# Performance work log

Hardware: AMD Instinct MI355X
Metric: run time of the kernel (lower is better)

## Reference

```python
import jax, jax.numpy as jnp
import numpy as np

H = 16
D_MODEL = 1024
D_K = D_MODEL // H  # 64
TEMP = float(np.sqrt(D_K))


def setup_inputs() -> dict:
    key = jax.random.key(0)
    ks = jax.random.split(key, 12)
    N = 2048
    s_in = 1.0 / np.sqrt(D_MODEL)
    inp = {
        "query": jax.random.normal(ks[0], (N, D_MODEL), jnp.float32),
        "key": jax.random.normal(ks[1], (N, D_MODEL), jnp.float32),
        "value": jax.random.normal(ks[2], (N, D_MODEL), jnp.float32),
        "Wq": jax.random.normal(ks[3], (D_MODEL, D_MODEL), jnp.float32) * s_in,
        "bq": jnp.zeros((D_MODEL,), jnp.float32),
        "Wk": jax.random.normal(ks[4], (D_MODEL, D_MODEL), jnp.float32) * s_in,
        "bk": jnp.zeros((D_MODEL,), jnp.float32),
        "Wv": jax.random.normal(ks[5], (D_MODEL, D_MODEL), jnp.float32) * s_in,
        "bv": jnp.zeros((D_MODEL,), jnp.float32),
        "Wo": jax.random.normal(ks[6], (D_MODEL, D_MODEL), jnp.float32) * s_in,
        "bo": jnp.zeros((D_MODEL,), jnp.float32),
    }
    return inp


def reference(query, key, value, Wq, bq, Wk, bk, Wv, bv, Wo, bo):
    # Project then split heads exactly like view(-1, h, d_k).transpose(0, 1):
    # (N, d_model) -> (N, h, d_k) -> (h, N, d_k)
    q = (query @ Wq + bq).reshape(-1, H, D_K).transpose(1, 0, 2)
    k = (key @ Wk + bk).reshape(-1, H, D_K).transpose(1, 0, 2)
    v = (value @ Wv + bv).reshape(-1, H, D_K).transpose(1, 0, 2)
    # Scaled dot-product attention (dropout is inference-mode identity)
    scores = jnp.einsum("hnd,hmd->hnm", q / TEMP, k)  # (h, N, N)
    attn = jax.nn.softmax(scores, axis=-1)
    x = jnp.einsum("hnm,hmd->hnd", attn, v)  # (h, N, d_k)
    x = x.transpose(1, 0, 2).reshape(-1, H * D_K)  # (N, d_model)
    out = x @ Wo + bo
    return (out, attn)
```

## Files before the change

### kernel.cpp

```cpp
#include <hip/hip_runtime.h>
#include <math.h>

#define NTOK 2048
#define DMODEL 1024
#define NHEAD 16
#define DHEAD 64
#define NTIL (NTOK / 64)

typedef _Float16 f16x8 __attribute__((ext_vector_type(8)));
typedef _Float16 f16x4 __attribute__((ext_vector_type(4)));
typedef _Float16 f16x2 __attribute__((ext_vector_type(2)));
typedef float f32x4 __attribute__((ext_vector_type(4)));
typedef float f32x16 __attribute__((ext_vector_type(16)));

union U32H2 { f16x2 h; unsigned u; };
union U8 { f16x8 v; unsigned u[4]; };

__device__ __forceinline__ void split16(float x, _Float16& hi, _Float16& lo) {
    hi = (_Float16)x;
    lo = (_Float16)(x - (float)hi);
}
__device__ __forceinline__ unsigned packh(_Float16 a, _Float16 b) {
    U32H2 c; c.h = f16x2{a, b}; return c.u;
}

__global__ void __launch_bounds__(256) prep_w_kernel(
        const float* __restrict__ Wq, const float* __restrict__ Wk,
        const float* __restrict__ Wv, const float* __restrict__ Wo,
        _Float16* __restrict__ Wt) {
    __shared__ float T[32][33];
    const int z = blockIdx.z;
    const float* W = (z == 0) ? Wq : (z == 1) ? Wk : (z == 2) ? Wv : Wo;
    _Float16* Whi = Wt + (size_t)z * 2 * 1024 * 1024;
    _Float16* Wlo = Whi + (size_t)1024 * 1024;
    const int t = threadIdx.x;
    const int k0 = blockIdx.y * 32, n0 = blockIdx.x * 32;
    const int r = t >> 3, c4 = (t & 7) * 4;
    const float4 v = *(const float4*)(W + (size_t)(k0 + r) * DMODEL + n0 + c4);
    T[r][c4 + 0] = v.x; T[r][c4 + 1] = v.y; T[r][c4 + 2] = v.z; T[r][c4 + 3] = v.w;
    __syncthreads();
    f16x4 hv, lv;
#pragma unroll
    for (int j = 0; j < 4; ++j) {
        _Float16 h, l;
        split16(T[c4 + j][r], h, l);
        hv[j] = h; lv[j] = l;
    }
    *(f16x4*)(Whi + (size_t)(n0 + r) * DMODEL + k0 + c4) = hv;
    *(f16x4*)(Wlo + (size_t)(n0 + r) * DMODEL + k0 + c4) = lv;
}

__global__ void __launch_bounds__(256) prep_a_kernel(
        const float* __restrict__ q, const float* __restrict__ k, const float* __restrict__ v,
        _Float16* __restrict__ As) {
    const int z = blockIdx.y;
    const float* A = (z == 0) ? q : (z == 1) ? k : v;
    const size_t PL = (size_t)NTOK * DMODEL;
    _Float16* H = As + (size_t)z * 2 * PL;
    _Float16* L = H + PL;
    const size_t off = ((size_t)blockIdx.x * 256 + threadIdx.x) * 8;
    const float4 a = *(const float4*)(A + off);
    const float4 b = *(const float4*)(A + off + 4);
    f16x8 hv, lv; _Float16 h, lo;
    split16(a.x, h, lo); hv[0] = h; lv[0] = lo;
    split16(a.y, h, lo); hv[1] = h; lv[1] = lo;
    split16(a.z, h, lo); hv[2] = h; lv[2] = lo;
    split16(a.w, h, lo); hv[3] = h; lv[3] = lo;
    split16(b.x, h, lo); hv[4] = h; lv[4] = lo;
    split16(b.y, h, lo); hv[5] = h; lv[5] = lo;
    split16(b.z, h, lo); hv[6] = h; lv[6] = lo;
    split16(b.w, h, lo); hv[7] = h; lv[7] = lo;
    *(f16x8*)(H + off) = hv;
    *(f16x8*)(L + off) = lv;
}

__global__ void __launch_bounds__(256) qkv_mfma_kernel(
        const _Float16* __restrict__ As,
        const _Float16* __restrict__ Wt,
        const float* __restrict__ bq, const float* __restrict__ bk, const float* __restrict__ bv,
        _Float16* __restrict__ Qh, _Float16* __restrict__ Ql,
        _Float16* __restrict__ Kh, _Float16* __restrict__ Vth) {
    __shared__ _Float16 Ah[64][40], Al[64][40], Bh[128][40], Bl[128][40];
    const int z = blockIdx.z;
    const size_t PL = (size_t)NTOK * DMODEL;
    const _Float16* AH = As + (size_t)z * 2 * PL;
    const _Float16* AL = AH + PL;
    const _Float16* WH = Wt + (size_t)z * 2 * 1024 * 1024;
    const _Float16* WL = WH + (size_t)1024 * 1024;
    const float* bias = (z == 0) ? bq : (z == 1) ? bk : bv;

    const int t = threadIdx.x;
    const int l = t & 63, wid = t >> 6;
    const int lr = l & 15, lk = l >> 4;
    const int m0 = blockIdx.y * 64, n0 = blockIdx.x * 128;
    const int wm = (wid >> 1) * 32, wn = (wid & 1) * 64;

    f32x4 acc[2][4];
#pragma unroll
    for (int mi = 0; mi < 2; ++mi)
#pragma unroll
        for (int ni = 0; ni < 4; ++ni)
#pragma unroll
            for (int e = 0; e < 4; ++e) acc[mi][ni][e] = 0.f;

    for (int k0 = 0; k0 < DMODEL; k0 += 32) {
        __syncthreads();
        {
            const int r = t >> 2, c8 = (t & 3) * 8;
            *(f16x8*)&Ah[r][c8] = *(const f16x8*)(AH + (size_t)(m0 + r) * DMODEL + k0 + c8);
            *(f16x8*)&Al[r][c8] = *(const f16x8*)(AL + (size_t)(m0 + r) * DMODEL + k0 + c8);
        }
#pragma unroll
        for (int p = 0; p < 2; ++p) {
            const int idx = t + p * 256;
            const int r = idx >> 2, c8 = (idx & 3) * 8;
            *(f16x8*)&Bh[r][c8] = *(const f16x8*)(WH + (size_t)(n0 + r) * DMODEL + k0 + c8);
            *(f16x8*)&Bl[r][c8] = *(const f16x8*)(WL + (size_t)(n0 + r) * DMODEL + k0 + c8);
        }
        __syncthreads();

        f16x8 ah[2], al[2], bh[4], bl[4];
#pragma unroll
        for (int i = 0; i < 2; ++i) {
            ah[i] = *(f16x8*)&Ah[wm + i * 16 + lr][lk * 8];
            al[i] = *(f16x8*)&Al[wm + i * 16 + lr][lk * 8];
        }
#pragma unroll
        for (int i = 0; i < 4; ++i) {
            bh[i] = *(f16x8*)&Bh[wn + i * 16 + lr][lk * 8];
            bl[i] = *(f16x8*)&Bl[wn + i * 16 + lr][lk * 8];
        }
        __builtin_amdgcn_s_setprio(1);
#pragma unroll
        for (int mi = 0; mi < 2; ++mi)
#pragma unroll
            for (int ni = 0; ni < 4; ++ni) {
                acc[mi][ni] = __builtin_amdgcn_mfma_f32_16x16x32_f16(ah[mi], bh[ni], acc[mi][ni], 0, 0, 0);
                acc[mi][ni] = __builtin_amdgcn_mfma_f32_16x16x32_f16(ah[mi], bl[ni], acc[mi][ni], 0, 0, 0);
                acc[mi][ni] = __builtin_amdgcn_mfma_f32_16x16x32_f16(al[mi], bh[ni], acc[mi][ni], 0, 0, 0);
            }
        __builtin_amdgcn_s_setprio(0);
    }

#pragma unroll
    for (int ni = 0; ni < 4; ++ni) {
        const int col = n0 + wn + ni * 16 + lr;
        const float bv_ = bias[col];
#pragma unroll
        for (int mi = 0; mi < 2; ++mi) {
            if (z == 2) {
                f16x4 hv;
#pragma unroll
                for (int i = 0; i < 4; ++i) hv[i] = (_Float16)(acc[mi][ni][i] + bv_);
                const int row = m0 + wm + mi * 16 + lk * 4;
                *(f16x4*)(Vth + (size_t)col * NTOK + row) = hv;
            } else {
#pragma unroll
                for (int i = 0; i < 4; ++i) {
                    const int row = m0 + wm + mi * 16 + lk * 4 + i;
                    float v = acc[mi][ni][i] + bv_;
                    if (z == 0) {
                        v *= 0.125f;
                        _Float16 h, lo;
                        split16(v, h, lo);
                        Qh[(size_t)row * DMODEL + col] = h;
                        Ql[(size_t)row * DMODEL + col] = lo;
                    } else {
                        Kh[(size_t)row * DMODEL + col] = (_Float16)v;
                    }
                }
            }
        }
    }
}

__global__ void __launch_bounds__(256, 2) fused_attn_kernel(
        const _Float16* __restrict__ Qh, const _Float16* __restrict__ Ql,
        const _Float16* __restrict__ Kh, const _Float16* __restrict__ Vth,
        float* __restrict__ attn, float* __restrict__ Xp) {
    __shared__ _Float16 KB[4][64][64];
    __shared__ _Float16 VB[4][64][64];
    const int t = threadIdx.x, l = t & 63, w = t >> 6, q = l & 31, h = l >> 5;
    const int hh = blockIdx.y;
    const int rw = blockIdx.x * 128 + w * 32;
    const int sr = t >> 3, sc = t & 7;
    const int qrow = rw + q;

    f16x8 qbh[4], qbl[4];
#pragma unroll
    for (int s = 0; s < 4; ++s) {
        const size_t off = (size_t)qrow * DMODEL + hh * DHEAD + s * 16 + h * 8;
        qbh[s] = *(const f16x8*)(Qh + off);
        qbl[s] = *(const f16x8*)(Ql + off);
    }

    auto stageK = [&](int buf, int j0) {
#pragma unroll
        for (int p = 0; p < 2; ++p) {
            const int r = sr + p * 32; const int cs = (sc ^ (r & 7)) * 8;
            *(f16x8*)&KB[buf][r][cs] = *(const f16x8*)(Kh + (size_t)(j0 + r) * DMODEL + hh * DHEAD + sc * 8);
        }
    };
    auto stageV = [&](int buf, int j0) {
#pragma unroll
        for (int p = 0; p < 2; ++p) {
            const int r = sr + p * 32; const int cs = (sc ^ (r & 7)) * 8;
            *(f16x8*)&VB[buf][r][cs] = *(const f16x8*)(Vth + (size_t)(hh * DHEAD + r) * NTOK + j0 + sc * 8);
        }
    };

    auto qkt = [&](int buf, f32x16 (&c)[2]) {
#pragma unroll
        for (int kb = 0; kb < 2; ++kb) {
#pragma unroll
            for (int r = 0; r < 16; ++r) c[kb][r] = 0.f;
            __builtin_amdgcn_s_setprio(1);
#pragma unroll
            for (int s = 0; s < 4; ++s) {
                const int rk = kb * 32 + q; const int cc = ((2 * s + h) ^ (rk & 7)) * 8;
                const f16x8 ah = *(f16x8*)&KB[buf][rk][cc];
                c[kb] = __builtin_amdgcn_mfma_f32_32x32x16_f16(ah, qbh[s], c[kb], 0, 0, 0);
                c[kb] = __builtin_amdgcn_mfma_f32_32x32x16_f16(ah, qbl[s], c[kb], 0, 0, 0);
            }
            __builtin_amdgcn_s_setprio(0);
        }
    };

    float lsum = 0.f;
    stageK(0, 0);
    stageK(1, 64);
    for (int it = 0; it < NTIL; it += 2) {
        __syncthreads();
        if (it + 2 < NTIL) stageK((it + 2) & 3, (it + 2) * 64);
        if (it + 3 < NTIL) stageK((it + 3) & 3, (it + 3) * 64);
#pragma unroll
        for (int u = 0; u < 2; ++u) {
            f32x16 c[2];
            qkt((it + u) & 3, c);
#pragma unroll
            for (int kb = 0; kb < 2; ++kb)
#pragma unroll
                for (int r = 0; r < 16; ++r) lsum += __expf(c[kb][r]);
        }
    }
    lsum += __shfl_xor(lsum, 32);
    const float linv = 1.f / lsum;

    f32x16 x0, x1;
#pragma unroll
    for (int r = 0; r < 16; ++r) { x0[r] = 0.f; x1[r] = 0.f; }

    __syncthreads();
    stageK(0, 0);  stageV(0, 0);
    stageK(1, 64); stageV(1, 64);
    for (int it = 0; it < NTIL; it += 2) {
        __syncthreads();
        if (it + 2 < NTIL) { stageK((it + 2) & 3, (it + 2) * 64); stageV((it + 2) & 3, (it + 2) * 64); }
        if (it + 3 < NTIL) { stageK((it + 3) & 3, (it + 3) * 64); stageV((it + 3) & 3, (it + 3) * 64); }
#pragma unroll
        for (int u = 0; u < 2; ++u) {
            const int cur = (it + u) & 3;
            const int j0 = (it + u) * 64;
            f32x16 c[2];
            qkt(cur, c);

#pragma unroll
            for (int kb = 0; kb < 2; ++kb) {
                float p[16];
#pragma unroll
                for (int r = 0; r < 16; ++r) p[r] = __expf(c[kb][r]) * linv;

                const int kbase = j0 + kb * 32;
#pragma unroll
                for (int i = 0; i < 4; ++i) {
                    f32x4 st;
                    st[0] = p[4 * i]; st[1] = p[4 * i + 1]; st[2] = p[4 * i + 2]; st[3] = p[4 * i + 3];
                    *(f32x4*)(attn + ((size_t)hh * NTOK + qrow) * NTOK + kbase + 8 * i + 4 * h) = st;
                }

                _Float16 hf[16];
#pragma unroll
                for (int r = 0; r < 16; ++r) hf[r] = (_Float16)p[r];
                unsigned ph[8];
#pragma unroll
                for (int i = 0; i < 8; ++i) ph[i] = packh(hf[2 * i], hf[2 * i + 1]);

#pragma unroll
                for (int ss = 0; ss < 2; ++ss) {
                    const int b = 4 * ss;
                    const unsigned eh0 = __shfl_xor(h ? ph[b + 0] : ph[b + 2], 32);
                    const unsigned eh1 = __shfl_xor(h ? ph[b + 1] : ph[b + 3], 32);
                    U8 pah;
                    pah.u[0] = h ? eh0 : ph[b + 0]; pah.u[1] = h ? eh1 : ph[b + 1];
                    pah.u[2] = h ? ph[b + 2] : eh0; pah.u[3] = h ? ph[b + 3] : eh1;
                    const int ks = kb * 2 + ss;
                    __builtin_amdgcn_s_setprio(1);
                    {
                        const int rd0 = q; const int cv0 = ((2 * ks + h) ^ (rd0 & 7)) * 8;
                        const f16x8 vh = *(f16x8*)&VB[cur][rd0][cv0];
                        x0 = __builtin_amdgcn_mfma_f32_32x32x16_f16(pah.v, vh, x0, 0, 0, 0);
                    }
                    {
                        const int rd1 = 32 + q; const int cv1 = ((2 * ks + h) ^ (rd1 & 7)) * 8;
                        const f16x8 vh = *(f16x8*)&VB[cur][rd1][cv1];
                        x1 = __builtin_amdgcn_mfma_f32_32x32x16_f16(pah.v, vh, x1, 0, 0, 0);
                    }
                    __builtin_amdgcn_s_setprio(0);
                }
            }
        }
    }

#pragma unroll
    for (int r = 0; r < 16; ++r) {
        const int qloc = (r & 3) + 8 * (r >> 2) + 4 * h;
        Xp[(size_t)(rw + qloc) * DMODEL + hh * DHEAD + q]      = x0[r];
        Xp[(size_t)(rw + qloc) * DMODEL + hh * DHEAD + 32 + q] = x1[r];
    }
}

__global__ void __launch_bounds__(256) out_mfma_kernel(
        const float* __restrict__ Xp,
        const _Float16* __restrict__ WH, const _Float16* __restrict__ WL,
        const float* __restrict__ bo, float* __restrict__ out) {
    __shared__ _Float16 Ah[64][40], Al[64][40], Bh[128][40], Bl[128][40];
    const int t = threadIdx.x;
    const int l = t & 63, wid = t >> 6;
    const int lr = l & 15, lk = l >> 4;
    const int m0 = blockIdx.y * 64, n0 = blockIdx.x * 128;
    const int wm = (wid >> 1) * 32, wn = (wid & 1) * 64;

    f32x4 acc[2][4];
#pragma unroll
    for (int mi = 0; mi < 2; ++mi)
#pragma unroll
        for (int ni = 0; ni < 4; ++ni)
#pragma unroll
            for (int e = 0; e < 4; ++e) acc[mi][ni][e] = 0.f;

    for (int k0 = 0; k0 < DMODEL; k0 += 32) {
        __syncthreads();
#pragma unroll
        for (int p = 0; p < 2; ++p) {
            const int idx = t + p * 256;
            const int r = idx >> 3, c4 = (idx & 7) * 4;
            const size_t off = (size_t)(m0 + r) * DMODEL + k0 + c4;
            const float4 v0 = *(const float4*)(Xp + off);
            f16x4 hv, lv; _Float16 h, lo;
            split16(v0.x, h, lo); hv[0] = h; lv[0] = lo;
            split16(v0.y, h, lo); hv[1] = h; lv[1] = lo;
            split16(v0.z, h, lo); hv[2] = h; lv[2] = lo;
            split16(v0.w, h, lo); hv[3] = h; lv[3] = lo;
            *(f16x4*)&Ah[r][c4] = hv;
            *(f16x4*)&Al[r][c4] = lv;
        }
#pragma unroll
        for (int p = 0; p < 2; ++p) {
            const int idx = t + p * 256;
            const int r = idx >> 2, c8 = (idx & 3) * 8;
            *(f16x8*)&Bh[r][c8] = *(const f16x8*)(WH + (size_t)(n0 + r) * DMODEL + k0 + c8);
            *(f16x8*)&Bl[r][c8] = *(const f16x8*)(WL + (size_t)(n0 + r) * DMODEL + k0 + c8);
        }
        __syncthreads();

        f16x8 ah[2], al[2], bh[4], bl[4];
#pragma unroll
        for (int i = 0; i < 2; ++i) {
            ah[i] = *(f16x8*)&Ah[wm + i * 16 + lr][lk * 8];
            al[i] = *(f16x8*)&Al[wm + i * 16 + lr][lk * 8];
        }
#pragma unroll
        for (int i = 0; i < 4; ++i) {
            bh[i] = *(f16x8*)&Bh[wn + i * 16 + lr][lk * 8];
            bl[i] = *(f16x8*)&Bl[wn + i * 16 + lr][lk * 8];
        }
        __builtin_amdgcn_s_setprio(1);
#pragma unroll
        for (int mi = 0; mi < 2; ++mi)
#pragma unroll
            for (int ni = 0; ni < 4; ++ni) {
                acc[mi][ni] = __builtin_amdgcn_mfma_f32_16x16x32_f16(ah[mi], bh[ni], acc[mi][ni], 0, 0, 0);
                acc[mi][ni] = __builtin_amdgcn_mfma_f32_16x16x32_f16(ah[mi], bl[ni], acc[mi][ni], 0, 0, 0);
                acc[mi][ni] = __builtin_amdgcn_mfma_f32_16x16x32_f16(al[mi], bh[ni], acc[mi][ni], 0, 0, 0);
            }
        __builtin_amdgcn_s_setprio(0);
    }

#pragma unroll
    for (int ni = 0; ni < 4; ++ni) {
        const int col = n0 + wn + ni * 16 + lr;
        const float bv_ = bo[col];
#pragma unroll
        for (int mi = 0; mi < 2; ++mi)
#pragma unroll
            for (int i = 0; i < 4; ++i) {
                const int row = m0 + wm + mi * 16 + lk * 4 + i;
                out[(size_t)row * DMODEL + col] = acc[mi][ni][i] + bv_;
            }
    }
}

extern "C" void kernel_launch(void* const* d_in, const int* in_sizes, int n_in,
                              void* d_out, int out_size, void* d_ws, size_t ws_size,
                              hipStream_t stream) {
    (void)in_sizes; (void)n_in; (void)out_size; (void)ws_size;
    const float* query = (const float*)d_in[0];
    const float* key_  = (const float*)d_in[1];
    const float* value = (const float*)d_in[2];
    const float* Wq = (const float*)d_in[3];
    const float* bq = (const float*)d_in[4];
    const float* Wk = (const float*)d_in[5];
    const float* bk = (const float*)d_in[6];
    const float* Wv = (const float*)d_in[7];
    const float* bv = (const float*)d_in[8];
    const float* Wo = (const float*)d_in[9];
    const float* bo = (const float*)d_in[10];

    float* out  = (float*)d_out;
    float* attn = out + (size_t)NTOK * DMODEL;

    const size_t MM = (size_t)1024 * 1024;
    _Float16* ws16 = (_Float16*)d_ws;
    _Float16* Wt  = ws16;
    _Float16* Qh  = ws16 + 8 * MM;
    _Float16* Ql  = Qh  + 2 * MM;
    _Float16* Kh_ = Ql  + 2 * MM;
    _Float16* Vth = Kh_ + 2 * MM;

    float* Xp = (float*)ws16;

    _Float16* As = (_Float16*)attn;

    dim3 blk(256);
    prep_w_kernel<<<dim3(32, 32, 4), blk, 0, stream>>>(Wq, Wk, Wv, Wo, Wt);
    prep_a_kernel<<<dim3(1024, 3), blk, 0, stream>>>(query, key_, value, As);
    qkv_mfma_kernel<<<dim3(8, 32, 3), blk, 0, stream>>>(As, Wt, bq, bk, bv,
                                                        Qh, Ql, Kh_, Vth);
    fused_attn_kernel<<<dim3(16, 16), blk, 0, stream>>>(Qh, Ql, Kh_, Vth, attn, Xp);
    out_mfma_kernel<<<dim3(8, 32), blk, 0, stream>>>(Xp, Wt + 6 * MM, Wt + 7 * MM, bo, out);
}
```

Measured before the change: 217.8 us.

## Split attention key range across two wave groups per block with LDS reduction

The fused attention kernel now launches 512 threads per block. Two groups of four waves each handle half of the key tiles for the same 128 query rows. Row sums and partial PV outputs are combined through shared memory. Each group double-buffers its own K/V tiles instead of using the previous 4-deep shared ring. This doubles the number of waves per block, raising occupancy and latency hiding with only 256 blocks on the grid, at the cost of extra barriers and a reduction step.

After: 216.4 us. About the same (-0.7%).

```diff
diff --git a/kernel.cpp b/kernel.cpp
--- a/kernel.cpp
+++ b/kernel.cpp
@@ -6,6 +6,7 @@
 #define NHEAD 16
 #define DHEAD 64
 #define NTIL (NTOK / 64)
+#define HTIL (NTIL / 2)
 
 typedef _Float16 f16x8 __attribute__((ext_vector_type(8)));
 typedef _Float16 f16x4 __attribute__((ext_vector_type(4)));
@@ -174,17 +175,20 @@
     }
 }
 
-__global__ void __launch_bounds__(256, 2) fused_attn_kernel(
+__global__ void __launch_bounds__(512, 2) fused_attn_kernel(
         const _Float16* __restrict__ Qh, const _Float16* __restrict__ Ql,
         const _Float16* __restrict__ Kh, const _Float16* __restrict__ Vth,
         float* __restrict__ attn, float* __restrict__ Xp) {
-    __shared__ _Float16 KB[4][64][64];
-    __shared__ _Float16 VB[4][64][64];
+    __shared__ _Float16 KB[2][2][64][64];
+    __shared__ _Float16 VB[2][2][64][64];
     const int t = threadIdx.x, l = t & 63, w = t >> 6, q = l & 31, h = l >> 5;
+    const int qsub = w & 3, kg = w >> 2;
     const int hh = blockIdx.y;
-    const int rw = blockIdx.x * 128 + w * 32;
-    const int sr = t >> 3, sc = t & 7;
+    const int rw = blockIdx.x * 128 + qsub * 32;
+    const int tg = t & 255;
+    const int sr = tg >> 3, sc = tg & 7;
     const int qrow = rw + q;
+    const int jb = kg * HTIL;
 
     f16x8 qbh[4], qbl[4];
 #pragma unroll
@@ -194,21 +198,22 @@
         qbl[s] = *(const f16x8*)(Ql + off);
     }
 
-    auto stageK = [&](int buf, int j0) {
+    auto stageK = [&](int buf, int tile) {
+        const int j0 = tile * 64;
 #pragma unroll
         for (int p = 0; p < 2; ++p) {
             const int r = sr + p * 32; const int cs = (sc ^ (r & 7)) * 8;
-            *(f16x8*)&KB[buf][r][cs] = *(const f16x8*)(Kh + (size_t)(j0 + r) * DMODEL + hh * DHEAD + sc * 8);
+            *(f16x8*)&KB[kg][buf][r][cs] = *(const f16x8*)(Kh + (size_t)(j0 + r) * DMODEL + hh * DHEAD + sc * 8);
         }
     };
-    auto stageV = [&](int buf, int j0) {
+    auto stageV = [&](int buf, int tile) {
+        const int j0 = tile * 64;
 #pragma unroll
         for (int p = 0; p < 2; ++p) {
             const int r = sr + p * 32; const int cs = (sc ^ (r & 7)) * 8;
-            *(f16x8*)&VB[buf][r][cs] = *(const f16x8*)(Vth + (size_t)(hh * DHEAD + r) * NTOK + j0 + sc * 8);
+            *(f16x8*)&VB[kg][buf][r][cs] = *(const f16x8*)(Vth + (size_t)(hh * DHEAD + r) * NTOK + j0 + sc * 8);
         }
     };
-
     auto qkt = [&](int buf, f32x16 (&c)[2]) {
 #pragma unroll
         for (int kb = 0; kb < 2; ++kb) {
@@ -218,7 +223,7 @@
 #pragma unroll
             for (int s = 0; s < 4; ++s) {
                 const int rk = kb * 32 + q; const int cc = ((2 * s + h) ^ (rk & 7)) * 8;
-                const f16x8 ah = *(f16x8*)&KB[buf][rk][cc];
+                const f16x8 ah = *(f16x8*)&KB[kg][buf][rk][cc];
                 c[kb] = __builtin_amdgcn_mfma_f32_32x32x16_f16(ah, qbh[s], c[kb], 0, 0, 0);
                 c[kb] = __builtin_amdgcn_mfma_f32_32x32x16_f16(ah, qbl[s], c[kb], 0, 0, 0);
             }
@@ -227,95 +232,108 @@
     };
 
     float lsum = 0.f;
-    stageK(0, 0);
-    stageK(1, 64);
-    for (int it = 0; it < NTIL; it += 2) {
-        __syncthreads();
-        if (it + 2 < NTIL) stageK((it + 2) & 3, (it + 2) * 64);
-        if (it + 3 < NTIL) stageK((it + 3) & 3, (it + 3) * 64);
-#pragma unroll
-        for (int u = 0; u < 2; ++u) {
-            f32x16 c[2];
-            qkt((it + u) & 3, c);
-#pragma unroll
-            for (int kb = 0; kb < 2; ++kb)
-#pragma unroll
-                for (int r = 0; r < 16; ++r) lsum += __expf(c[kb][r]);
-        }
+    stageK(0, jb);
+    for (int it = 0; it < HTIL; ++it) {
+        __syncthreads();
+        if (it + 1 < HTIL) stageK((it + 1) & 1, jb + it + 1);
+        f32x16 c[2];
+        qkt(it & 1, c);
+#pragma unroll
+        for (int kb = 0; kb < 2; ++kb)
+#pragma unroll
+            for (int r = 0; r < 16; ++r) lsum += __expf(c[kb][r]);
     }
     lsum += __shfl_xor(lsum, 32);
-    const float linv = 1.f / lsum;
+
+    float* ls = (float*)VB;
+    if (h == 0) ls[w * 32 + q] = lsum;
+    __syncthreads();
+    const float linv = 1.f / (ls[qsub * 32 + q] + ls[(qsub + 4) * 32 + q]);
+    __syncthreads();
 
     f32x16 x0, x1;
 #pragma unroll
     for (int r = 0; r < 16; ++r) { x0[r] = 0.f; x1[r] = 0.f; }
 
+    stageK(0, jb);
+    stageV(0, jb);
+    for (int it = 0; it < HTIL; ++it) {
+        const int j0 = (jb + it) * 64;
+        __syncthreads();
+        const int cur = it & 1;
+        if (it + 1 < HTIL) { stageK(cur ^ 1, jb + it + 1); stageV(cur ^ 1, jb + it + 1); }
+
+        f32x16 c[2];
+        qkt(cur, c);
+
+#pragma unroll
+        for (int kb = 0; kb < 2; ++kb) {
+            float p[16];
+#pragma unroll
+            for (int r = 0; r < 16; ++r) p[r] = __expf(c[kb][r]) * linv;
+
+            const int kbase = j0 + kb * 32;
+#pragma unroll
+            for (int i = 0; i < 4; ++i) {
+                f32x4 st;
+                st[0] = p[4 * i]; st[1] = p[4 * i + 1]; st[2] = p[4 * i + 2]; st[3] = p[4 * i + 3];
+                *(f32x4*)(attn + ((size_t)hh * NTOK + qrow) * NTOK + kbase + 8 * i + 4 * h) = st;
+            }
+
+            _Float16 hf[16];
+#pragma unroll
+            for (int r = 0; r < 16; ++r) hf[r] = (_Float16)p[r];
+            unsigned ph[8];
+#pragma unroll
+            for (int i = 0; i < 8; ++i) ph[i] = packh(hf[2 * i], hf[2 * i + 1]);
+
+#pragma unroll
+            for (int ss = 0; ss < 2; ++ss) {
+                const int b = 4 * ss;
+                const unsigned eh0 = __shfl_xor(h ? ph[b + 0] : ph[b + 2], 32);
+                const unsigned eh1 = __shfl_xor(h ? ph[b + 1] : ph[b + 3], 32);
+                U8 pah;
+                pah.u[0] = h ? eh0 : ph[b + 0]; pah.u[1] = h ? eh1 : ph[b + 1];
+                pah.u[2] = h ? ph[b + 2] : eh0; pah.u[3] = h ? ph[b + 3] : eh1;
+                const int ks = kb * 2 + ss;
+                __builtin_amdgcn_s_setprio(1);
+                {
+                    const int rd0 = q; const int cv0 = ((2 * ks + h) ^ (rd0 & 7)) * 8;
+                    const f16x8 vh = *(f16x8*)&VB[kg][cur][rd0][cv0];
+                    x0 = __builtin_amdgcn_mfma_f32_32x32x16_f16(pah.v, vh, x0, 0, 0, 0);
+                }
+                {
+                    const int rd1 = 32 + q; const int cv1 = ((2 * ks + h) ^ (rd1 & 7)) * 8;
+                    const f16x8 vh = *(f16x8*)&VB[kg][cur][rd1][cv1];
+                    x1 = __builtin_amdgcn_mfma_f32_32x32x16_f16(pah.v, vh, x1, 0, 0, 0);
+                }
+                __builtin_amdgcn_s_setprio(0);
+            }
+        }
+    }
+
     __syncthreads();
-    stageK(0, 0);  stageV(0, 0);
-    stageK(1, 64); stageV(1, 64);
-    for (int it = 0; it < NTIL; it += 2) {
-        __syncthreads();
-        if (it + 2 < NTIL) { stageK((it + 2) & 3, (it + 2) * 64); stageV((it + 2) & 3, (it + 2) * 64); }
-        if (it + 3 < NTIL) { stageK((it + 3) & 3, (it + 3) * 64); stageV((it + 3) & 3, (it + 3) * 64); }
-#pragma unroll
-        for (int u = 0; u < 2; ++u) {
-            const int cur = (it + u) & 3;
-            const int j0 = (it + u) * 64;
-            f32x16 c[2];
-            qkt(cur, c);
-
-#pragma unroll
-            for (int kb = 0; kb < 2; ++kb) {
-                float p[16];
-#pragma unroll
-                for (int r = 0; r < 16; ++r) p[r] = __expf(c[kb][r]) * linv;
-
-                const int kbase = j0 + kb * 32;
-#pragma unroll
-                for (int i = 0; i < 4; ++i) {
-                    f32x4 st;
-                    st[0] = p[4 * i]; st[1] = p[4 * i + 1]; st[2] = p[4 * i + 2]; st[3] = p[4 * i + 3];
-                    *(f32x4*)(attn + ((size_t)hh * NTOK + qrow) * NTOK + kbase + 8 * i + 4 * h) = st;
-                }
-
-                _Float16 hf[16];
-#pragma unroll
-                for (int r = 0; r < 16; ++r) hf[r] = (_Float16)p[r];
-                unsigned ph[8];
-#pragma unroll
-                for (int i = 0; i < 8; ++i) ph[i] = packh(hf[2 * i], hf[2 * i + 1]);
-
-#pragma unroll
-                for (int ss = 0; ss < 2; ++ss) {
-                    const int b = 4 * ss;
-                    const unsigned eh0 = __shfl_xor(h ? ph[b + 0] : ph[b + 2], 32);
-                    const unsigned eh1 = __shfl_xor(h ? ph[b + 1] : ph[b + 3], 32);
-                    U8 pah;
-                    pah.u[0] = h ? eh0 : ph[b + 0]; pah.u[1] = h ? eh1 : ph[b + 1];
-                    pah.u[2] = h ? ph[b + 2] : eh0; pah.u[3] = h ? ph[b + 3] : eh1;
-                    const int ks = kb * 2 + ss;
-                    __builtin_amdgcn_s_setprio(1);
-                    {
-                        const int rd0 = q; const int cv0 = ((2 * ks + h) ^ (rd0 & 7)) * 8;
-                        const f16x8 vh = *(f16x8*)&VB[cur][rd0][cv0];
-                        x0 = __builtin_amdgcn_mfma_f32_32x32x16_f16(pah.v, vh, x0, 0, 0, 0);
-                    }
-                    {
-                        const int rd1 = 32 + q; const int cv1 = ((2 * ks + h) ^ (rd1 & 7)) * 8;
-                        const f16x8 vh = *(f16x8*)&VB[cur][rd1][cv1];
-                        x1 = __builtin_amdgcn_mfma_f32_32x32x16_f16(pah.v, vh, x1, 0, 0, 0);
-                    }
-                    __builtin_amdgcn_s_setprio(0);
-                }
-            }
-        }
-    }
-
-#pragma unroll
-    for (int r = 0; r < 16; ++r) {
-        const int qloc = (r & 3) + 8 * (r >> 2) + 4 * h;
-        Xp[(size_t)(rw + qloc) * DMODEL + hh * DHEAD + q]      = x0[r];
-        Xp[(size_t)(rw + qloc) * DMODEL + hh * DHEAD + 32 + q] = x1[r];
+    float* xs = (float*)KB;
+    if (kg == 1) {
+#pragma unroll
+        for (int r = 0; r < 16; ++r) {
+            xs[((qsub * 64) + l) * 32 + r]      = x0[r];
+            xs[((qsub * 64) + l) * 32 + 16 + r] = x1[r];
+        }
+    }
+    __syncthreads();
+    if (kg == 0) {
+#pragma unroll
+        for (int r = 0; r < 16; ++r) {
+            x0[r] += xs[((qsub * 64) + l) * 32 + r];
+            x1[r] += xs[((qsub * 64) + l) * 32 + 16 + r];
+        }
+#pragma unroll
+        for (int r = 0; r < 16; ++r) {
+            const int qloc = (r & 3) + 8 * (r >> 2) + 4 * h;
+            Xp[(size_t)(rw + qloc) * DMODEL + hh * DHEAD + q]      = x0[r];
+            Xp[(size_t)(rw + qloc) * DMODEL + hh * DHEAD + 32 + q] = x1[r];
+        }
     }
 }
 
@@ -436,6 +454,6 @@
     prep_a_kernel<<<dim3(1024, 3), blk, 0, stream>>>(query, key_, value, As);
     qkv_mfma_kernel<<<dim3(8, 32, 3), blk, 0, stream>>>(As, Wt, bq, bk, bv,
                                                         Qh, Ql, Kh_, Vth);
-    fused_attn_kernel<<<dim3(16, 16), blk, 0, stream>>>(Qh, Ql, Kh_, Vth, attn, Xp);
+    fused_attn_kernel<<<dim3(16, 16), dim3(512), 0, stream>>>(Qh, Ql, Kh_, Vth, attn, Xp);
     out_mfma_kernel<<<dim3(8, 32), blk, 0, stream>>>(Xp, Wt + 6 * MM, Wt + 7 * MM, bo, out);
 }
```
